# Kernel tuning notes

Measured on AMD Instinct MI355X. Metric: run time of the kernel, lower is better.

The kernel has to match this reference:

```python
import jax, jax.numpy as jnp
import numpy as np

IN, OUT, IO, CF, CS = 128, 128, 512, 512, 1024
B = 8192
TAU_IO, TAU_CF, TAU_CS = 2.0, 5.0, 70.0


def _lin(x, W, b):
    # torch nn.Linear: y = x @ W.T + b, W has shape [out, in]
    return x @ W.T + b


def setup_inputs() -> dict:
    key = jax.random.key(0)
    ks = jax.random.split(key, 24)

    def wb(i, fan_out, fan_in):
        s = 1.0 / np.sqrt(fan_in)
        W = jax.random.uniform(ks[2 * i], (fan_out, fan_in), jnp.float32, -s, s)
        b = jax.random.uniform(ks[2 * i + 1], (fan_out,), jnp.float32, -s, s)
        return W, b

    Wi2io, bi2io = wb(0, IO, IN)
    Wio2o, bio2o = wb(1, OUT, IO)
    Wio2io, bio2io = wb(2, IO, IO)
    Wio2cf, bio2cf = wb(3, CF, IO)
    Wcf2io, bcf2io = wb(4, IO, CF)
    Wcf2cs, bcf2cs = wb(5, CS, CF)
    Wcf2cf, bcf2cf = wb(6, CF, CF)
    Wcs2cf, bcs2cf = wb(7, CF, CS)
    Wcs2cs, bcs2cs = wb(8, CS, CS)

    x = jax.random.normal(ks[18], (B, IN), jnp.float32)
    io_state = jnp.zeros((B, IO), jnp.float32)
    cf_state = jnp.zeros((B, CF), jnp.float32)
    cs_state = jnp.zeros((B, CS), jnp.float32)

    return dict(
        x=x, io_state=io_state, cf_state=cf_state, cs_state=cs_state,
        Wi2io=Wi2io, bi2io=bi2io, Wio2o=Wio2o, bio2o=bio2o,
        Wio2io=Wio2io, bio2io=bio2io, Wio2cf=Wio2cf, bio2cf=bio2cf,
        Wcf2io=Wcf2io, bcf2io=bcf2io, Wcf2cs=Wcf2cs, bcf2cs=bcf2cs,
        Wcf2cf=Wcf2cf, bcf2cf=bcf2cf, Wcs2cf=Wcs2cf, bcs2cf=bcs2cf,
        Wcs2cs=Wcs2cs, bcs2cs=bcs2cs,
    )


def reference(x, io_state, cf_state, cs_state,
              Wi2io, bi2io, Wio2o, bio2o,
              Wio2io, bio2io, Wio2cf, bio2cf,
              Wcf2io, bcf2io, Wcf2cs, bcf2cs,
              Wcf2cf, bcf2cf, Wcs2cf, bcs2cf,
              Wcs2cs, bcs2cs):
    x = x.reshape(-1, IN)
    # leaky-integrated updates; all branches read the *previous* states
    io_new = jnp.tanh(
        (1.0 - 1.0 / TAU_IO) * io_state
        + (_lin(io_state, Wio2io, bio2io)
           + _lin(cf_state, Wcf2io, bcf2io)
           + _lin(x, Wi2io, bi2io)) / TAU_IO)
    cf_new = jnp.tanh(
        (1.0 - 1.0 / TAU_CF) * cf_state
        + (_lin(cf_state, Wcf2cf, bcf2cf)
           + _lin(cs_state, Wcs2cf, bcs2cf)
           + _lin(io_state, Wio2cf, bio2cf)) / TAU_CF)
    cs_new = jnp.tanh(
        (1.0 - 1.0 / TAU_CS) * cs_state
        + (_lin(cs_state, Wcs2cs, bcs2cs)
           + _lin(cf_state, Wcf2cs, bcf2cs)) / TAU_CS)
    y = jnp.tanh(_lin(io_new, Wio2o, bio2o))
    return y
```

## Files before the change

kernel.cpp:

```cpp
#include <hip/hip_runtime.h>


typedef float f32x4 __attribute__((ext_vector_type(4)));
typedef __bf16 bf16x4 __attribute__((ext_vector_type(4)));
typedef __bf16 bf16x8 __attribute__((ext_vector_type(8)));
typedef unsigned short u16x4 __attribute__((ext_vector_type(4)));

__device__ __forceinline__ unsigned short f2bf(float f) {
    unsigned u = __builtin_bit_cast(unsigned, f);
    u += 0x7FFFu + ((u >> 16) & 1u);
    return (unsigned short)(u >> 16);
}

__device__ __forceinline__ float tanh_fast(float x) {
    float e = __expf(2.0f * x);
    return 1.0f - 2.0f * __builtin_amdgcn_rcpf(e + 1.0f);
}

__device__ __forceinline__ void gload16(const void* g, void* l) {
    __builtin_amdgcn_global_load_lds(
        (const __attribute__((address_space(1))) void*)g,
        (__attribute__((address_space(3))) void*)l, 16, 0, 0);
}

__device__ __forceinline__ void wait_barrier() {
    asm volatile("s_waitcnt vmcnt(0)\n\ts_barrier" ::: "memory");
}

__global__ __launch_bounds__(256) void k_convert(
    const float* __restrict__ Wi2io, const float* __restrict__ Wio2io,
    const float* __restrict__ Wcf2io, const float* __restrict__ Wio2o,
    const float* __restrict__ b1, const float* __restrict__ b2,
    const float* __restrict__ b3,
    unsigned short* __restrict__ wcat, unsigned short* __restrict__ w2s,
    float* __restrict__ bsum)
{
    int idx = blockIdx.x * 256 + threadIdx.x;
    if (idx < 147456) {
        int n = idx / 288;
        int k = (idx - n * 288) * 4;
        const float* s;
        if (k < 128)      s = Wi2io  + n * 128 + k;
        else if (k < 640) s = Wio2io + n * 512 + (k - 128);
        else              s = Wcf2io + n * 512 + (k - 640);
        f32x4 v = *(const f32x4*)s;
        u16x4 h;
        #pragma unroll
        for (int t = 0; t < 4; ++t) {
            float f = 0.5f * v[t];
            int kk = k + t;
            if (kk >= 128 && kk < 640 && (kk - 128) == n) f += 0.5f;
            h[t] = f2bf(f);
        }
        int ad = n * 1152 + (k & ~63) + ((((k >> 3) & 7) ^ (n & 7)) << 3) + (k & 7);
        *(u16x4*)(wcat + ad) = h;
    } else if (idx < 163840) {
        int q = idx - 147456;
        int n = q >> 7;
        int k = (q & 127) * 4;
        f32x4 v = *(const f32x4*)(Wio2o + n * 512 + k);
        u16x4 h; h[0]=f2bf(v[0]); h[1]=f2bf(v[1]); h[2]=f2bf(v[2]); h[3]=f2bf(v[3]);
        int ad = n * 512 + (k & ~63) + ((((k >> 3) & 7) ^ (n & 7)) << 3) + (k & 7);
        *(u16x4*)(w2s + ad) = h;
    } else if (idx < 164352) {
        int n = idx - 163840;
        bsum[n] = 0.5f * (b1[n] + b2[n] + b3[n]);
    }
}

__global__ __launch_bounds__(512, 2) void k_gemm1(
    const float* __restrict__ x, const float* __restrict__ io,
    const float* __restrict__ cf,
    const unsigned short* __restrict__ wcat,
    const float* __restrict__ bsum,
    unsigned short* __restrict__ ionew)
{
    __shared__ __align__(16) char lds[2][49152];

    const int tid = threadIdx.x, b = blockIdx.x;
    const int xcd = b & 7, idx = b >> 3;
    const int m0 = ((xcd << 4) | (idx & 15)) << 6;
    const int n0 = (idx >> 4) << 8;

    const int lane = tid & 63, wid = tid >> 6;
    const int li = lane & 15, lh = lane >> 4;
    const int wm = (wid >> 2) << 5;
    const int wn = (wid & 3) << 6;

    int a_off_x[2], a_off_s[2], b_off[4];
    #pragma unroll
    for (int j = 0; j < 2; ++j) {
        int r = (wid << 3) + (j << 2) + (lane >> 4);
        int cs = ((lane & 15) ^ (r & 15)) << 2;
        a_off_x[j] = (m0 + r) * 128 + cs;
        a_off_s[j] = (m0 + r) * 512 + cs;
    }
    #pragma unroll
    for (int j = 0; j < 4; ++j) {
        int rb = (wid << 5) + (j << 3) + (lane >> 3);
        b_off[j] = (n0 + rb) * 1152 + ((lane & 7) << 3);
    }
    const int adstA = wid << 11;
    const int adstB = wid << 12;

    f32x4 zz = {0.f, 0.f, 0.f, 0.f};
    f32x4 acc[2][4];
    #pragma unroll
    for (int i = 0; i < 2; ++i)
        #pragma unroll
        for (int j = 0; j < 4; ++j) acc[i][j] = zz;

#define STAGE1(KT, BUF) do {                                                   \
        int K_ = (KT);                                                         \
        char* A_ = (BUF); char* B_ = (BUF) + 16384;                            \
        if (K_ < 2) {                                                          \
            const float* sp = x + (K_ << 6);                                   \
            _Pragma("unroll")                                                  \
            for (int j = 0; j < 2; ++j)                                        \
                gload16(sp + a_off_x[j], A_ + adstA + (j << 10));              \
        } else if (K_ < 10) {                                                  \
            const float* sp = io + ((K_ - 2) << 6);                            \
            _Pragma("unroll")                                                  \
            for (int j = 0; j < 2; ++j)                                        \
                gload16(sp + a_off_s[j], A_ + adstA + (j << 10));              \
        } else {                                                               \
            const float* sp = cf + ((K_ - 10) << 6);                           \
            _Pragma("unroll")                                                  \
            for (int j = 0; j < 2; ++j)                                        \
                gload16(sp + a_off_s[j], A_ + adstA + (j << 10));              \
        }                                                                      \
        const unsigned short* wp = wcat + (K_ << 6);                           \
        _Pragma("unroll")                                                      \
        for (int j = 0; j < 4; ++j)                                            \
            gload16(wp + b_off[j], B_ + adstB + (j << 10));                    \
    } while (0)

#define COMPUTE1(BUF) do {                                                     \
        const char* A_ = (BUF); const char* B_ = (BUF) + 16384;                \
        _Pragma("unroll")                                                      \
        for (int ks = 0; ks < 2; ++ks) {                                       \
            bf16x8 af[2];                                                      \
            _Pragma("unroll")                                                  \
            for (int mi = 0; mi < 2; ++mi) {                                   \
                int r = wm + mi * 16 + li;                                     \
                int c0 = ks * 8 + lh * 2;                                      \
                f32x4 a0 = *(const f32x4*)(A_ + r * 256 +                      \
                                           ((c0 ^ (r & 15)) << 4));            \
                f32x4 a1 = *(const f32x4*)(A_ + r * 256 +                      \
                                           (((c0 + 1) ^ (r & 15)) << 4));      \
                bf16x4 h0 = __builtin_convertvector(a0, bf16x4);               \
                bf16x4 h1 = __builtin_convertvector(a1, bf16x4);               \
                af[mi] = __builtin_shufflevector(h0, h1, 0,1,2,3,4,5,6,7);     \
            }                                                                  \
            _Pragma("unroll")                                                  \
            for (int nj = 0; nj < 4; ++nj) {                                   \
                int rb = wn + nj * 16 + li;                                    \
                int cb = ks * 4 + lh;                                          \
                bf16x8 bv = *(const bf16x8*)(B_ + rb * 128 +                   \
                                             ((cb ^ (rb & 7)) << 4));          \
                acc[0][nj] = __builtin_amdgcn_mfma_f32_16x16x32_bf16(          \
                    af[0], bv, acc[0][nj], 0, 0, 0);                           \
                acc[1][nj] = __builtin_amdgcn_mfma_f32_16x16x32_bf16(          \
                    af[1], bv, acc[1][nj], 0, 0, 0);                           \
            }                                                                  \
        }                                                                      \
    } while (0)

    STAGE1(0, lds[0]);
    wait_barrier();
    #pragma unroll 1
    for (int kt = 0; kt < 18; ++kt) {
        if (kt + 1 < 18) STAGE1(kt + 1, lds[(kt + 1) & 1]);
        COMPUTE1(lds[kt & 1]);
        wait_barrier();
    }
#undef STAGE1
#undef COMPUTE1

    #pragma unroll
    for (int nj = 0; nj < 4; ++nj) {
        int gn = n0 + wn + nj * 16 + li;
        float bb = bsum[gn];
        #pragma unroll
        for (int mi = 0; mi < 2; ++mi) {
            #pragma unroll
            for (int r = 0; r < 4; ++r) {
                int gm = m0 + wm + mi * 16 + (lh << 2) + r;
                float v = tanh_fast(acc[mi][nj][r] + bb);
                int ad = gm * 512 + (gn & ~63) +
                         ((((gn >> 3) & 7) ^ (gm & 7)) << 3) + (gn & 7);
                ionew[ad] = f2bf(v);
            }
        }
    }
}

__global__ __launch_bounds__(256, 2) void k_gemm2(
    const unsigned short* __restrict__ ionew,
    const unsigned short* __restrict__ w2s,
    const float* __restrict__ b4,
    float* __restrict__ out)
{
    __shared__ __align__(16) char lds[2][20480];

    const int tid = threadIdx.x, b = blockIdx.x;
    const int xcd = b & 7, idx = b >> 3;
    const int m0 = ((xcd << 5) | idx) << 5;

    const int lane = tid & 63, wid = tid >> 6;
    const int li = lane & 15, lh = lane >> 4;
    const int wn = wid << 5;

    const int a2_off = (m0 + (wid << 3) + (lane >> 3)) * 512 + ((lane & 7) << 3);
    int b2_off[4];
    #pragma unroll
    for (int j = 0; j < 4; ++j)
        b2_off[j] = ((wid << 5) + 8 * j + (lane >> 3)) * 512 + ((lane & 7) << 3);

    f32x4 zz = {0.f, 0.f, 0.f, 0.f};
    f32x4 acc[2][2];
    acc[0][0] = zz; acc[0][1] = zz; acc[1][0] = zz; acc[1][1] = zz;

#define STAGE2(KT, BUF) do {                                                   \
        int K_ = (KT);                                                         \
        char* A_ = (BUF); char* B_ = (BUF) + 4096;                             \
        gload16(ionew + a2_off + (K_ << 6), A_ + (wid << 10));                 \
        _Pragma("unroll")                                                      \
        for (int j = 0; j < 4; ++j)                                            \
            gload16(w2s + b2_off[j] + (K_ << 6), B_ + (wid << 12) + j * 1024); \
    } while (0)

#define COMPUTE2(BUF) do {                                                     \
        const char* A_ = (BUF); const char* B_ = (BUF) + 4096;                 \
        _Pragma("unroll")                                                      \
        for (int ks = 0; ks < 2; ++ks) {                                       \
            int c = ks * 4 + lh;                                               \
            bf16x8 av[2];                                                      \
            _Pragma("unroll")                                                  \
            for (int mi = 0; mi < 2; ++mi) {                                   \
                int r = mi * 16 + li;                                          \
                av[mi] = *(const bf16x8*)(A_ + r * 128 + ((c ^ (r & 7)) << 4));\
            }                                                                  \
            _Pragma("unroll")                                                  \
            for (int nj = 0; nj < 2; ++nj) {                                   \
                int rb = wn + nj * 16 + li;                                    \
                bf16x8 bv = *(const bf16x8*)(B_ + rb * 128 +                   \
                                             ((c ^ (rb & 7)) << 4));           \
                acc[0][nj] = __builtin_amdgcn_mfma_f32_16x16x32_bf16(          \
                    av[0], bv, acc[0][nj], 0, 0, 0);                           \
                acc[1][nj] = __builtin_amdgcn_mfma_f32_16x16x32_bf16(          \
                    av[1], bv, acc[1][nj], 0, 0, 0);                           \
            }                                                                  \
        }                                                                      \
    } while (0)

    STAGE2(0, lds[0]);
    wait_barrier();
    #pragma unroll 1
    for (int kt = 0; kt < 8; ++kt) {
        if (kt + 1 < 8) STAGE2(kt + 1, lds[(kt + 1) & 1]);
        COMPUTE2(lds[kt & 1]);
        wait_barrier();
    }
#undef STAGE2
#undef COMPUTE2

    #pragma unroll
    for (int nj = 0; nj < 2; ++nj) {
        int n = wn + nj * 16 + li;
        float bb = b4[n];
        #pragma unroll
        for (int mi = 0; mi < 2; ++mi) {
            #pragma unroll
            for (int r = 0; r < 4; ++r) {
                int gm = m0 + mi * 16 + (lh << 2) + r;
                out[(size_t)gm * 128 + n] = tanh_fast(acc[mi][nj][r] + bb);
            }
        }
    }
}

extern "C" void kernel_launch(void* const* d_in, const int* in_sizes, int n_in,
                              void* d_out, int out_size, void* d_ws, size_t ws_size,
                              hipStream_t stream)
{
    const float* x      = (const float*)d_in[0];
    const float* io     = (const float*)d_in[1];
    const float* cf     = (const float*)d_in[2];
    const float* Wi2io  = (const float*)d_in[4];
    const float* bi2io  = (const float*)d_in[5];
    const float* Wio2o  = (const float*)d_in[6];
    const float* bio2o  = (const float*)d_in[7];
    const float* Wio2io = (const float*)d_in[8];
    const float* bio2io = (const float*)d_in[9];
    const float* Wcf2io = (const float*)d_in[12];
    const float* bcf2io = (const float*)d_in[13];
    float* out = (float*)d_out;

    char* ws = (char*)d_ws;
    unsigned short* wcat  = (unsigned short*)ws;
    unsigned short* w2s   = (unsigned short*)(ws + 1179648);
    float*          bsum  = (float*)(ws + 1310720);
    unsigned short* ionew = (unsigned short*)(ws + 1312768);

    hipLaunchKernelGGL(k_convert, dim3(642), dim3(256), 0, stream,
                       Wi2io, Wio2io, Wcf2io, Wio2o, bi2io, bio2io, bcf2io,
                       wcat, w2s, bsum);
    hipLaunchKernelGGL(k_gemm1, dim3(256), dim3(512), 0, stream,
                       x, io, cf, wcat, bsum, ionew);
    hipLaunchKernelGGL(k_gemm2, dim3(256), dim3(256), 0, stream,
                       ionew, w2s, bio2o, out);
}
```

Before: 37.40 us.

## Triple-buffer both GEMM pipelines with partial vmcnt waits and retile GEMM1 to 128x128

Both GEMM kernels move from double to triple LDS buffering. Each iteration now waits only for the oldest outstanding stage (vmcnt 6 or 5) rather than draining every load, so two tiles stay in flight while one is computed. GEMM1's block tile also changes from 64x256 to 128x128 with a matching wave layout and per-wave load split. This trades more LDS per block, which lowers possible occupancy in GEMM1, for better latency hiding and a squarer tile.

New measurement: 32.88 us. 1.14x faster.

```diff
diff --git a/kernel.cpp b/kernel.cpp
--- a/kernel.cpp
+++ b/kernel.cpp
@@ -23,9 +23,7 @@
         (__attribute__((address_space(3))) void*)l, 16, 0, 0);
 }
 
-__device__ __forceinline__ void wait_barrier() {
-    asm volatile("s_waitcnt vmcnt(0)\n\ts_barrier" ::: "memory");
-}
+#define WAITB(N) asm volatile("s_waitcnt vmcnt(" #N ")\n\ts_barrier" ::: "memory")
 
 __global__ __launch_bounds__(256) void k_convert(
     const float* __restrict__ Wi2io, const float* __restrict__ Wio2io,
@@ -75,33 +73,33 @@
     const float* __restrict__ bsum,
     unsigned short* __restrict__ ionew)
 {
-    __shared__ __align__(16) char lds[2][49152];
+    __shared__ __align__(16) char lds[3][49152];
 
     const int tid = threadIdx.x, b = blockIdx.x;
     const int xcd = b & 7, idx = b >> 3;
-    const int m0 = ((xcd << 4) | (idx & 15)) << 6;
-    const int n0 = (idx >> 4) << 8;
+    const int m0 = ((xcd << 3) | (idx & 7)) << 7;
+    const int n0 = (idx >> 3) << 7;
 
     const int lane = tid & 63, wid = tid >> 6;
     const int li = lane & 15, lh = lane >> 4;
-    const int wm = (wid >> 2) << 5;
-    const int wn = (wid & 3) << 6;
-
-    int a_off_x[2], a_off_s[2], b_off[4];
-    #pragma unroll
-    for (int j = 0; j < 2; ++j) {
-        int r = (wid << 3) + (j << 2) + (lane >> 4);
+    const int wm = (wid >> 1) << 5;
+    const int wn = (wid & 1) << 6;
+
+    int a_off_x[4], a_off_s[4], b_off[2];
+    #pragma unroll
+    for (int j = 0; j < 4; ++j) {
+        int r = (wid << 4) + (j << 2) + (lane >> 4);
         int cs = ((lane & 15) ^ (r & 15)) << 2;
         a_off_x[j] = (m0 + r) * 128 + cs;
         a_off_s[j] = (m0 + r) * 512 + cs;
     }
     #pragma unroll
-    for (int j = 0; j < 4; ++j) {
-        int rb = (wid << 5) + (j << 3) + (lane >> 3);
+    for (int j = 0; j < 2; ++j) {
+        int rb = ((wid << 1) + j) * 8 + (lane >> 3);
         b_off[j] = (n0 + rb) * 1152 + ((lane & 7) << 3);
     }
-    const int adstA = wid << 11;
-    const int adstB = wid << 12;
+    const int adstA = wid << 12;
+    const int adstB = wid << 11;
 
     f32x4 zz = {0.f, 0.f, 0.f, 0.f};
     f32x4 acc[2][4];
@@ -112,31 +110,31 @@
 
 #define STAGE1(KT, BUF) do {                                                   \
         int K_ = (KT);                                                         \
-        char* A_ = (BUF); char* B_ = (BUF) + 16384;                            \
+        char* A_ = (BUF); char* B_ = (BUF) + 32768;                            \
         if (K_ < 2) {                                                          \
             const float* sp = x + (K_ << 6);                                   \
             _Pragma("unroll")                                                  \
-            for (int j = 0; j < 2; ++j)                                        \
+            for (int j = 0; j < 4; ++j)                                        \
                 gload16(sp + a_off_x[j], A_ + adstA + (j << 10));              \
         } else if (K_ < 10) {                                                  \
             const float* sp = io + ((K_ - 2) << 6);                            \
             _Pragma("unroll")                                                  \
-            for (int j = 0; j < 2; ++j)                                        \
+            for (int j = 0; j < 4; ++j)                                        \
                 gload16(sp + a_off_s[j], A_ + adstA + (j << 10));              \
         } else {                                                               \
             const float* sp = cf + ((K_ - 10) << 6);                           \
             _Pragma("unroll")                                                  \
-            for (int j = 0; j < 2; ++j)                                        \
+            for (int j = 0; j < 4; ++j)                                        \
                 gload16(sp + a_off_s[j], A_ + adstA + (j << 10));              \
         }                                                                      \
         const unsigned short* wp = wcat + (K_ << 6);                           \
         _Pragma("unroll")                                                      \
-        for (int j = 0; j < 4; ++j)                                            \
+        for (int j = 0; j < 2; ++j)                                            \
             gload16(wp + b_off[j], B_ + adstB + (j << 10));                    \
     } while (0)
 
 #define COMPUTE1(BUF) do {                                                     \
-        const char* A_ = (BUF); const char* B_ = (BUF) + 16384;                \
+        const char* A_ = (BUF); const char* B_ = (BUF) + 32768;                \
         _Pragma("unroll")                                                      \
         for (int ks = 0; ks < 2; ++ks) {                                       \
             bf16x8 af[2];                                                      \
@@ -167,13 +165,17 @@
     } while (0)
 
     STAGE1(0, lds[0]);
-    wait_barrier();
+    STAGE1(1, lds[1]);
+    char* p0 = lds[0]; char* p1 = lds[1]; char* p2 = lds[2];
     #pragma unroll 1
-    for (int kt = 0; kt < 18; ++kt) {
-        if (kt + 1 < 18) STAGE1(kt + 1, lds[(kt + 1) & 1]);
-        COMPUTE1(lds[kt & 1]);
-        wait_barrier();
-    }
+    for (int t = 0; t < 17; ++t) {
+        WAITB(6);
+        if (t + 2 < 18) STAGE1(t + 2, p2);
+        COMPUTE1(p0);
+        char* tmp = p0; p0 = p1; p1 = p2; p2 = tmp;
+    }
+    WAITB(0);
+    COMPUTE1(p0);
 #undef STAGE1
 #undef COMPUTE1
 
@@ -201,7 +203,7 @@
     const float* __restrict__ b4,
     float* __restrict__ out)
 {
-    __shared__ __align__(16) char lds[2][20480];
+    __shared__ __align__(16) char lds[3][20480];
 
     const int tid = threadIdx.x, b = blockIdx.x;
     const int xcd = b & 7, idx = b >> 3;
@@ -255,13 +257,17 @@
     } while (0)
 
     STAGE2(0, lds[0]);
-    wait_barrier();
+    STAGE2(1, lds[1]);
+    char* p0 = lds[0]; char* p1 = lds[1]; char* p2 = lds[2];
     #pragma unroll 1
-    for (int kt = 0; kt < 8; ++kt) {
-        if (kt + 1 < 8) STAGE2(kt + 1, lds[(kt + 1) & 1]);
-        COMPUTE2(lds[kt & 1]);
-        wait_barrier();
-    }
+    for (int t = 0; t < 7; ++t) {
+        WAITB(5);
+        if (t + 2 < 8) STAGE2(t + 2, p2);
+        COMPUTE2(p0);
+        char* tmp = p0; p0 = p1; p1 = p2; p2 = tmp;
+    }
+    WAITB(0);
+    COMPUTE2(p0);
 #undef STAGE2
 #undef COMPUTE2
 
```
